# Optimization experiments

Hardware: AMD Instinct MI355X
Metric: run time of the kernel (lower is better)

Reference implementation:

```python
import jax, jax.numpy as jnp
import numpy as np

N_NODES = 100000
N_EDGES = 1600000
H, D, DE = 4, 32, 32  # heads, node_out_feats, edge_out_feats
NEG_SLOPE = 0.2


def setup_inputs() -> dict:
    key = jax.random.key(0)
    ks = jax.random.split(key, 10)
    return {
        "node_inputs": jax.random.normal(ks[0], (N_NODES, 128), jnp.float32),
        "edge_inputs": jax.random.normal(ks[1], (N_EDGES, 16), jnp.float32),
        "src": jax.random.randint(ks[2], (N_EDGES,), 0, N_NODES, jnp.int32),
        "dst": jax.random.randint(ks[3], (N_EDGES,), 0, N_NODES, jnp.int32),
        "W_fc": jax.random.normal(ks[4], (128, H * D), jnp.float32) * 0.1,
        "attn_src_p": jax.random.normal(ks[5], (1, H, D), jnp.float32) * 0.1,
        "attn_dst_p": jax.random.normal(ks[6], (1, H, D), jnp.float32) * 0.1,
        "W_edge": jax.random.normal(ks[7], (16, H * DE), jnp.float32) * 0.1,
        "attn_edge_p": jax.random.normal(ks[8], (1, H, DE), jnp.float32) * 0.1,
        "W_res": jax.random.normal(ks[9], (128, H * D), jnp.float32) * 0.1,
        "bias_p": jnp.zeros((H * D,), jnp.float32),
    }


def reference(node_inputs, edge_inputs, src, dst, W_fc, attn_src_p,
              attn_dst_p, W_edge, attn_edge_p, W_res, bias_p):
    N = node_inputs.shape[0]
    # node projection: [N, H, D]
    feat = (node_inputs @ W_fc).reshape(N, H, D)
    # per-node attention logits [N, H]
    a_src = (feat * attn_src_p).sum(-1)
    a_dst = (feat * attn_dst_p).sum(-1)
    # edge-feature attention logits [E, H]
    feat_e = (edge_inputs @ W_edge).reshape(-1, H, DE)
    a_edge = (feat_e * attn_edge_p).sum(-1)
    # per-edge score: u_add_v + edge term, then LeakyReLU
    e = a_src[src] + a_dst[dst] + a_edge                 # [E, H]
    e = jnp.where(e > 0, e, NEG_SLOPE * e)
    # edge softmax grouped by destination node
    emax = jax.lax.stop_gradient(jax.ops.segment_max(e, dst, num_segments=N))
    ex = jnp.exp(e - emax[dst])
    denom = jax.ops.segment_sum(ex, dst, num_segments=N)
    attn = ex / denom[dst]                               # [E, H]
    # weighted scatter-aggregate of source features
    msg = feat[src] * attn[:, :, None]                   # [E, H, D]
    x = jax.ops.segment_sum(msg, dst, num_segments=N)    # [N, H, D]
    # residual + bias
    x = x + (node_inputs @ W_res).reshape(N, H, D)
    x = x + bias_p.reshape(H, D)
    return x
```

## Files before the change

kernel.cpp:

```cpp
#include <hip/hip_runtime.h>
#include <math.h>

#define NNODES_FEAT 128
#define HD 128
#define H 4
#define D 32
#define EDGE_F 16
#define NEG_SLOPE 0.2f

typedef _Float16 f16;
typedef _Float16 f16x2 __attribute__((ext_vector_type(2)));
typedef _Float16 f16x4 __attribute__((ext_vector_type(4)));
typedef _Float16 f16x8 __attribute__((ext_vector_type(8)));
typedef float f32x4 __attribute__((ext_vector_type(4)));

union ExPack { float2 f; f16x4 h; };

__global__ void k_wedge(const float* __restrict__ W_edge,
                        const float* __restrict__ attn_edge,
                        float* __restrict__ w_eh) {
    int t = threadIdx.x;
    int k = t >> 2;
    int h = t & 3;
    float s = 0.f;
    for (int d = 0; d < D; ++d)
        s += W_edge[k * HD + h * D + d] * attn_edge[h * D + d];
    w_eh[k * H + h] = s;
}

__global__ __launch_bounds__(256) void k_wt(const float* __restrict__ Wfc,
                                            const float* __restrict__ Wres,
                                            f16* __restrict__ Wt) {
    int i = blockIdx.x * 256 + threadIdx.x;
    int n = i >> 7, k = i & 127;
    float v = (n < 128) ? Wfc[k * HD + n] : Wres[k * HD + (n - 128)];
    Wt[(size_t)n * 128 + k] = (f16)v;
}

#define LDK 136
__global__ __launch_bounds__(256) void k_gemm_mfma(
    const float* __restrict__ A, const f16* __restrict__ Wt,
    const float* __restrict__ bias, f16* __restrict__ feat16,
    float* __restrict__ out, int N) {
    __shared__ f16 As[64 * LDK];
    __shared__ f16 Bs[128 * LDK];
    int tid = threadIdx.x;
    int wave = tid >> 6, lane = tid & 63;
    int m0 = blockIdx.x * 64;

    for (int c = tid; c < 64 * 32; c += 256) {
        int r = c >> 5, cc = (c & 31) * 4;
        int gr = m0 + r;
        float4 v = make_float4(0.f, 0.f, 0.f, 0.f);
        if (gr < N) v = *(const float4*)(A + (size_t)gr * 128 + cc);
        f16x4 h = {(f16)v.x, (f16)v.y, (f16)v.z, (f16)v.w};
        *(f16x4*)(&As[r * LDK + cc]) = h;
    }

    int am = lane & 15, aq = lane >> 4;
    int arow = wave * 16 + am;
    int orow0 = m0 + wave * 16 + aq * 4;

    for (int cb = 0; cb < 2; ++cb) {
        if (cb) __syncthreads();
        const f16* Wblk = Wt + (size_t)cb * 128 * 128;
        for (int c = tid; c < 128 * 16; c += 256) {
            int r = c >> 4, cc = (c & 15) * 8;
            float4 v = *(const float4*)(Wblk + (size_t)r * 128 + cc);
            *(float4*)(&Bs[r * LDK + cc]) = v;
        }
        __syncthreads();

        f32x4 acc[8];
#pragma unroll
        for (int nt = 0; nt < 8; ++nt) acc[nt] = (f32x4){0.f, 0.f, 0.f, 0.f};
#pragma unroll
        for (int kc = 0; kc < 4; ++kc) {
            f16x8 a = *(const f16x8*)(&As[arow * LDK + kc * 32 + aq * 8]);
#pragma unroll
            for (int nt = 0; nt < 8; ++nt) {
                f16x8 b = *(const f16x8*)(&Bs[(nt * 16 + am) * LDK + kc * 32 + aq * 8]);
                acc[nt] = __builtin_amdgcn_mfma_f32_16x16x32_f16(a, b, acc[nt], 0, 0, 0);
            }
        }

        if (cb == 0) {
#pragma unroll
            for (int nt = 0; nt < 8; ++nt) {
                int col = nt * 16 + am;
#pragma unroll
                for (int r = 0; r < 4; ++r) {
                    int row = orow0 + r;
                    if (row < N) feat16[(size_t)row * 128 + col] = (f16)acc[nt][r];
                }
            }
        } else {
#pragma unroll
            for (int nt = 0; nt < 8; ++nt) {
                int col = nt * 16 + am;
                float bv = bias[col];
#pragma unroll
                for (int r = 0; r < 4; ++r) {
                    int row = orow0 + r;
                    if (row < N) out[(size_t)row * 128 + col] = acc[nt][r] + bv;
                }
            }
        }
    }
}

__global__ __launch_bounds__(256) void k_attn_nodes(
    const f16* __restrict__ feat16, const float* __restrict__ attn_src,
    const float* __restrict__ attn_dst, float* __restrict__ a_src,
    float* __restrict__ a_dst, int N) {
    int g = blockIdx.x * 256 + threadIdx.x;
    int n = g >> 2, h = g & 3;
    if (n >= N) return;
    const f16* f = feat16 + (size_t)n * HD + h * D;
    const float* w1 = attn_src + h * D;
    const float* w2 = attn_dst + h * D;
    float s1 = 0.f, s2 = 0.f;
#pragma unroll
    for (int dd = 0; dd < D; dd += 8) {
        f16x8 fv = *(const f16x8*)(f + dd);
#pragma unroll
        for (int j = 0; j < 8; ++j) {
            float fx = (float)fv[j];
            s1 += fx * w1[dd + j];
            s2 += fx * w2[dd + j];
        }
    }
    a_src[n * H + h] = s1;
    a_dst[n * H + h] = s2;
}

__global__ __launch_bounds__(256) void k_edge_logit(
    const float* __restrict__ edge_inputs, const int* __restrict__ src,
    const int* __restrict__ dst, const float* __restrict__ w_eh,
    const float* __restrict__ a_src, const float* __restrict__ a_dst,
    int* __restrict__ deg, int* __restrict__ rank,
    float2* __restrict__ evp, int E) {
    __shared__ float weh_s[EDGE_F * H];
    if (threadIdx.x < EDGE_F * H) weh_s[threadIdx.x] = w_eh[threadIdx.x];
    __syncthreads();

    int base = blockIdx.x * 512 + threadIdx.x;
    int e0 = base, e1 = base + 256;
    bool v0 = e0 < E, v1 = e1 < E;

    int s0 = v0 ? src[e0] : 0, s1 = v1 ? src[e1] : 0;
    int d0 = v0 ? dst[e0] : 0, d1 = v1 ? dst[e1] : 0;

    float4 xa[4], xb[4];
    if (v0) {
        const float* x = edge_inputs + (size_t)e0 * EDGE_F;
        xa[0] = *(const float4*)(x);      xa[1] = *(const float4*)(x + 4);
        xa[2] = *(const float4*)(x + 8);  xa[3] = *(const float4*)(x + 12);
    }
    if (v1) {
        const float* x = edge_inputs + (size_t)e1 * EDGE_F;
        xb[0] = *(const float4*)(x);      xb[1] = *(const float4*)(x + 4);
        xb[2] = *(const float4*)(x + 8);  xb[3] = *(const float4*)(x + 12);
    }

    float4 as0 = *(const float4*)(a_src + s0 * H);
    float4 ad0 = *(const float4*)(a_dst + d0 * H);
    float4 as1 = *(const float4*)(a_src + s1 * H);
    float4 ad1 = *(const float4*)(a_dst + d1 * H);

    int r0 = v0 ? atomicAdd(deg + d0, 1) : 0;
    int r1 = v1 ? atomicAdd(deg + d1, 1) : 0;

    if (v0) {
        float ae0 = 0.f, ae1 = 0.f, ae2 = 0.f, ae3 = 0.f;
        const float* xs = (const float*)xa;
#pragma unroll
        for (int k = 0; k < EDGE_F; ++k) {
            float xv = xs[k];
            ae0 += xv * weh_s[k * H + 0];
            ae1 += xv * weh_s[k * H + 1];
            ae2 += xv * weh_s[k * H + 2];
            ae3 += xv * weh_s[k * H + 3];
        }
        float ev[H];
        ev[0] = as0.x + ad0.x + ae0;
        ev[1] = as0.y + ad0.y + ae1;
        ev[2] = as0.z + ad0.z + ae2;
        ev[3] = as0.w + ad0.w + ae3;
#pragma unroll
        for (int h = 0; h < H; ++h) {
            float t = ev[h];
            t = t > 0.f ? t : NEG_SLOPE * t;
            ev[h] = __expf(t);
        }
        ExPack p;
        p.h = (f16x4){(f16)ev[0], (f16)ev[1], (f16)ev[2], (f16)ev[3]};
        evp[e0] = p.f;
        rank[e0] = r0;
    }
    if (v1) {
        float ae0 = 0.f, ae1 = 0.f, ae2 = 0.f, ae3 = 0.f;
        const float* xs = (const float*)xb;
#pragma unroll
        for (int k = 0; k < EDGE_F; ++k) {
            float xv = xs[k];
            ae0 += xv * weh_s[k * H + 0];
            ae1 += xv * weh_s[k * H + 1];
            ae2 += xv * weh_s[k * H + 2];
            ae3 += xv * weh_s[k * H + 3];
        }
        float ev[H];
        ev[0] = as1.x + ad1.x + ae0;
        ev[1] = as1.y + ad1.y + ae1;
        ev[2] = as1.z + ad1.z + ae2;
        ev[3] = as1.w + ad1.w + ae3;
#pragma unroll
        for (int h = 0; h < H; ++h) {
            float t = ev[h];
            t = t > 0.f ? t : NEG_SLOPE * t;
            ev[h] = __expf(t);
        }
        ExPack p;
        p.h = (f16x4){(f16)ev[0], (f16)ev[1], (f16)ev[2], (f16)ev[3]};
        evp[e1] = p.f;
        rank[e1] = r1;
    }
}

__global__ __launch_bounds__(256) void k_scan_partial(
    const int* __restrict__ deg, int* __restrict__ partial, int N) {
    __shared__ int sdata[256];
    int t = threadIdx.x;
    int base = blockIdx.x * 1024 + t * 4;
    int s = 0;
#pragma unroll
    for (int j = 0; j < 4; ++j) { int i = base + j; if (i < N) s += deg[i]; }
    sdata[t] = s;
    __syncthreads();
    for (int off = 128; off > 0; off >>= 1) {
        if (t < off) sdata[t] += sdata[t + off];
        __syncthreads();
    }
    if (t == 0) partial[blockIdx.x] = sdata[0];
}

__global__ __launch_bounds__(256) void k_scan_top(
    int* __restrict__ partial, int* __restrict__ offs, int nb, int N) {
    __shared__ int sdata[256];
    int t = threadIdx.x;
    int v = (t < nb) ? partial[t] : 0;
    sdata[t] = v;
    __syncthreads();
    for (int off = 1; off < 256; off <<= 1) {
        int add = (t >= off) ? sdata[t - off] : 0;
        __syncthreads();
        sdata[t] += add;
        __syncthreads();
    }
    int excl = (t == 0) ? 0 : sdata[t - 1];
    if (t < nb) partial[t] = excl;
    if (t == nb - 1) offs[N] = sdata[t];
}

__global__ __launch_bounds__(256) void k_scan_final(
    int* __restrict__ deg_offs, const int* __restrict__ partial, int N) {
    __shared__ int sdata[256];
    int t = threadIdx.x;
    int base = blockIdx.x * 1024 + t * 4;
    int v[4]; int s = 0;
#pragma unroll
    for (int j = 0; j < 4; ++j) { int i = base + j; v[j] = (i < N) ? deg_offs[i] : 0; s += v[j]; }
    sdata[t] = s;
    __syncthreads();
    for (int off = 1; off < 256; off <<= 1) {
        int add = (t >= off) ? sdata[t - off] : 0;
        __syncthreads();
        sdata[t] += add;
        __syncthreads();
    }
    int excl = partial[blockIdx.x] + ((t == 0) ? 0 : sdata[t - 1]);
#pragma unroll
    for (int j = 0; j < 4; ++j) {
        int i = base + j;
        if (i < N) { deg_offs[i] = excl; excl += v[j]; }
    }
}

__global__ __launch_bounds__(256) void k_permute(
    const int* __restrict__ src, const int* __restrict__ dst,
    const int* __restrict__ rank, const float2* __restrict__ evp,
    const int* __restrict__ offs, f32x4* __restrict__ rec, int E) {
    int base = blockIdx.x * 1024 + threadIdx.x;
    int s[4], d[4], r[4]; float2 q[4]; bool v[4];
#pragma unroll
    for (int j = 0; j < 4; ++j) {
        int e = base + j * 256;
        v[j] = e < E;
        s[j] = v[j] ? src[e] : 0;
        d[j] = v[j] ? dst[e] : 0;
        r[j] = v[j] ? rank[e] : 0;
        q[j] = v[j] ? evp[e] : make_float2(0.f, 0.f);
    }
    int pos[4];
#pragma unroll
    for (int j = 0; j < 4; ++j) pos[j] = offs[d[j]] + r[j];
#pragma unroll
    for (int j = 0; j < 4; ++j) {
        if (!v[j]) continue;
        f32x4 rr;
        rr[0] = __int_as_float(s[j]);
        rr[1] = q[j].x;
        rr[2] = q[j].y;
        rr[3] = 0.f;
        __builtin_nontemporal_store(rr, &rec[pos[j]]);
    }
}

__device__ __forceinline__ float exsel(float a, float b, int hword, int hshift) {
    unsigned u = __float_as_uint(hword ? b : a);
    unsigned short us = (unsigned short)(u >> hshift);
    f16 hv;
    __builtin_memcpy(&hv, &us, 2);
    return (float)hv;
}

__global__ __launch_bounds__(256) void k_aggr(
    const f16* __restrict__ feat16, const f32x4* __restrict__ rec,
    const int* __restrict__ offs, float* __restrict__ out, int N) {
    int wave = threadIdx.x >> 6;
    int lane = threadIdx.x & 63;
    int n = blockIdx.x * 4 + wave;
    if (n >= N) return;
    int beg = offs[n], end = offs[n + 1];
    if (end <= beg) return;
    int half = lane >> 5;
    int l = lane & 31;
    int hword = (l >> 4) & 1;
    int hshift = ((l >> 3) & 1) * 16;
    size_t c0 = (size_t)l * 4;
    float num0 = 0.f, num1 = 0.f, num2 = 0.f, num3 = 0.f, den = 0.f;
    int i = beg;
    for (; i + 3 < end; i += 4) {
        f32x4 ra = __builtin_nontemporal_load(&rec[i + half]);
        f32x4 rb = __builtin_nontemporal_load(&rec[i + 2 + half]);
        int sa = __float_as_int(ra[0]), sb = __float_as_int(rb[0]);
        f16x4 fa = *(const f16x4*)(feat16 + (size_t)sa * HD + c0);
        f16x4 fb = *(const f16x4*)(feat16 + (size_t)sb * HD + c0);
        float ea = exsel(ra[1], ra[2], hword, hshift);
        float eb = exsel(rb[1], rb[2], hword, hshift);
        num0 += ea * (float)fa[0] + eb * (float)fb[0];
        num1 += ea * (float)fa[1] + eb * (float)fb[1];
        num2 += ea * (float)fa[2] + eb * (float)fb[2];
        num3 += ea * (float)fa[3] + eb * (float)fb[3];
        den  += ea + eb;
    }
    for (; i + 1 < end; i += 2) {
        f32x4 ra = __builtin_nontemporal_load(&rec[i + half]);
        int sa = __float_as_int(ra[0]);
        f16x4 fa = *(const f16x4*)(feat16 + (size_t)sa * HD + c0);
        float ea = exsel(ra[1], ra[2], hword, hshift);
        num0 += ea * (float)fa[0];
        num1 += ea * (float)fa[1];
        num2 += ea * (float)fa[2];
        num3 += ea * (float)fa[3];
        den += ea;
    }
    if (i < end) {
        f32x4 ra = __builtin_nontemporal_load(&rec[i]);
        int sa = __float_as_int(ra[0]);
        f16x4 fa = *(const f16x4*)(feat16 + (size_t)sa * HD + c0);
        float ea = half ? 0.f : exsel(ra[1], ra[2], hword, hshift);
        num0 += ea * (float)fa[0];
        num1 += ea * (float)fa[1];
        num2 += ea * (float)fa[2];
        num3 += ea * (float)fa[3];
        den += ea;
    }
    num0 += __shfl_xor(num0, 32);
    num1 += __shfl_xor(num1, 32);
    num2 += __shfl_xor(num2, 32);
    num3 += __shfl_xor(num3, 32);
    den  += __shfl_xor(den, 32);
    if (half == 0) {
        float inv = 1.f / den;
        float* o = out + (size_t)n * HD + c0;
        float4 v = *(float4*)o;
        v.x += num0 * inv;
        v.y += num1 * inv;
        v.z += num2 * inv;
        v.w += num3 * inv;
        *(float4*)o = v;
    }
}

extern "C" void kernel_launch(void* const* d_in, const int* in_sizes, int n_in,
                              void* d_out, int out_size, void* d_ws, size_t ws_size,
                              hipStream_t stream) {
    const float* node_inputs = (const float*)d_in[0];
    const float* edge_inputs = (const float*)d_in[1];
    const int*   src         = (const int*)d_in[2];
    const int*   dst         = (const int*)d_in[3];
    const float* W_fc        = (const float*)d_in[4];
    const float* attn_src_p  = (const float*)d_in[5];
    const float* attn_dst_p  = (const float*)d_in[6];
    const float* W_edge      = (const float*)d_in[7];
    const float* attn_edge_p = (const float*)d_in[8];
    const float* W_res       = (const float*)d_in[9];
    const float* bias_p      = (const float*)d_in[10];

    int N = in_sizes[0] / NNODES_FEAT;
    int E = in_sizes[2];

    float* out = (float*)d_out;

    f16*    feat16  = (f16*)d_ws;
    f32x4*  rec     = (f32x4*)(feat16 + (size_t)N * HD);
    f16*    Wt      = (f16*)(rec + (size_t)E);
    float*  a_src   = (float*)(Wt + 256 * 128);
    float*  a_dst   = a_src + (size_t)N * H;
    float*  w_eh    = a_dst + (size_t)N * H;
    int*    deg     = (int*)(w_eh + 64);
    int*    offs    = deg;
    int*    partial = deg + (N + 2);
    int*    rank    = partial + 128;
    float2* evp     = (float2*)(rank + (size_t)E);

    hipMemsetAsync(deg, 0, (size_t)(N + 2) * sizeof(int), stream);

    k_wedge<<<1, 64, 0, stream>>>(W_edge, attn_edge_p, w_eh);
    k_wt<<<(256 * 128) / 256, 256, 0, stream>>>(W_fc, W_res, Wt);

    int gb = (N + 63) / 64;
    k_gemm_mfma<<<gb, 256, 0, stream>>>(node_inputs, Wt, bias_p, feat16, out, N);

    int nb = (N * H + 255) / 256;
    k_attn_nodes<<<nb, 256, 0, stream>>>(feat16, attn_src_p, attn_dst_p, a_src, a_dst, N);

    int eb = (E + 511) / 512;
    k_edge_logit<<<eb, 256, 0, stream>>>(edge_inputs, src, dst, w_eh, a_src, a_dst,
                                         deg, rank, evp, E);

    int sb = (N + 1023) / 1024;
    k_scan_partial<<<sb, 256, 0, stream>>>(deg, partial, N);
    k_scan_top<<<1, 256, 0, stream>>>(partial, offs, sb, N);
    k_scan_final<<<sb, 256, 0, stream>>>(deg, partial, N);

    int pb = (E + 1023) / 1024;
    k_permute<<<pb, 256, 0, stream>>>(src, dst, rank, evp, offs, rec, E);

    int ab = (N + 3) / 4;
    k_aggr<<<ab, 256, 0, stream>>>(feat16, rec, offs, out, N);
}
```

Before: 485.7 us.

## Fuse node attention logits into GEMM epilogue and restructure aggregation per wave

```diff
diff --git a/kernel.cpp b/kernel.cpp
--- a/kernel.cpp
+++ b/kernel.cpp
@@ -40,7 +40,9 @@
 #define LDK 136
 __global__ __launch_bounds__(256) void k_gemm_mfma(
     const float* __restrict__ A, const f16* __restrict__ Wt,
-    const float* __restrict__ bias, f16* __restrict__ feat16,
+    const float* __restrict__ bias, const float* __restrict__ asp,
+    const float* __restrict__ adp, f16* __restrict__ feat16,
+    float* __restrict__ a_src, float* __restrict__ a_dst,
     float* __restrict__ out, int N) {
     __shared__ f16 As[64 * LDK];
     __shared__ f16 Bs[128 * LDK];
@@ -94,6 +96,42 @@
                     if (row < N) feat16[(size_t)row * 128 + col] = (f16)acc[nt][r];
                 }
             }
+            float w1v[8], w2v[8];
+#pragma unroll
+            for (int nt = 0; nt < 8; ++nt) {
+                w1v[nt] = asp[nt * 16 + am];
+                w2v[nt] = adp[nt * 16 + am];
+            }
+#pragma unroll
+            for (int r = 0; r < 4; ++r) {
+                float p1[4] = {0.f, 0.f, 0.f, 0.f};
+                float p2[4] = {0.f, 0.f, 0.f, 0.f};
+#pragma unroll
+                for (int nt = 0; nt < 8; ++nt) {
+                    int h = nt >> 1;
+                    p1[h] += acc[nt][r] * w1v[nt];
+                    p2[h] += acc[nt][r] * w2v[nt];
+                }
+#pragma unroll
+                for (int off = 1; off < 16; off <<= 1) {
+#pragma unroll
+                    for (int h = 0; h < 4; ++h) {
+                        p1[h] += __shfl_xor(p1[h], off);
+                        p2[h] += __shfl_xor(p2[h], off);
+                    }
+                }
+                int row = orow0 + r;
+                if (row < N) {
+                    if (am < 4) {
+                        float v = am == 0 ? p1[0] : am == 1 ? p1[1] : am == 2 ? p1[2] : p1[3];
+                        a_src[row * 4 + am] = v;
+                    } else if (am < 8) {
+                        int hh = am - 4;
+                        float v = hh == 0 ? p2[0] : hh == 1 ? p2[1] : hh == 2 ? p2[2] : p2[3];
+                        a_dst[row * 4 + hh] = v;
+                    }
+                }
+            }
         } else {
 #pragma unroll
             for (int nt = 0; nt < 8; ++nt) {
@@ -107,31 +145,6 @@
             }
         }
     }
-}
-
-__global__ __launch_bounds__(256) void k_attn_nodes(
-    const f16* __restrict__ feat16, const float* __restrict__ attn_src,
-    const float* __restrict__ attn_dst, float* __restrict__ a_src,
-    float* __restrict__ a_dst, int N) {
-    int g = blockIdx.x * 256 + threadIdx.x;
-    int n = g >> 2, h = g & 3;
-    if (n >= N) return;
-    const f16* f = feat16 + (size_t)n * HD + h * D;
-    const float* w1 = attn_src + h * D;
-    const float* w2 = attn_dst + h * D;
-    float s1 = 0.f, s2 = 0.f;
-#pragma unroll
-    for (int dd = 0; dd < D; dd += 8) {
-        f16x8 fv = *(const f16x8*)(f + dd);
-#pragma unroll
-        for (int j = 0; j < 8; ++j) {
-            float fx = (float)fv[j];
-            s1 += fx * w1[dd + j];
-            s2 += fx * w2[dd + j];
-        }
-    }
-    a_src[n * H + h] = s1;
-    a_dst[n * H + h] = s2;
 }
 
 __global__ __launch_bounds__(256) void k_edge_logit(
@@ -289,7 +302,7 @@
 __global__ __launch_bounds__(256) void k_permute(
     const int* __restrict__ src, const int* __restrict__ dst,
     const int* __restrict__ rank, const float2* __restrict__ evp,
-    const int* __restrict__ offs, f32x4* __restrict__ rec, int E) {
+    const int* __restrict__ offs, float4* __restrict__ rec, int E) {
     int base = blockIdx.x * 1024 + threadIdx.x;
     int s[4], d[4], r[4]; float2 q[4]; bool v[4];
 #pragma unroll
@@ -307,12 +320,12 @@
 #pragma unroll
     for (int j = 0; j < 4; ++j) {
         if (!v[j]) continue;
-        f32x4 rr;
-        rr[0] = __int_as_float(s[j]);
-        rr[1] = q[j].x;
-        rr[2] = q[j].y;
-        rr[3] = 0.f;
-        __builtin_nontemporal_store(rr, &rec[pos[j]]);
+        float4 rr;
+        rr.x = __int_as_float(s[j]);
+        rr.y = q[j].x;
+        rr.z = q[j].y;
+        rr.w = 0.f;
+        rec[pos[j]] = rr;
     }
 }
 
@@ -325,7 +338,7 @@
 }
 
 __global__ __launch_bounds__(256) void k_aggr(
-    const f16* __restrict__ feat16, const f32x4* __restrict__ rec,
+    const f16* __restrict__ feat16, const float4* __restrict__ rec,
     const int* __restrict__ offs, float* __restrict__ out, int N) {
     int wave = threadIdx.x >> 6;
     int lane = threadIdx.x & 63;
@@ -333,64 +346,42 @@
     if (n >= N) return;
     int beg = offs[n], end = offs[n + 1];
     if (end <= beg) return;
-    int half = lane >> 5;
-    int l = lane & 31;
-    int hword = (l >> 4) & 1;
-    int hshift = ((l >> 3) & 1) * 16;
-    size_t c0 = (size_t)l * 4;
-    float num0 = 0.f, num1 = 0.f, num2 = 0.f, num3 = 0.f, den = 0.f;
+    int hword = (lane >> 5) & 1;
+    int hshift = ((lane >> 4) & 1) * 16;
+    size_t c0 = (size_t)2 * lane;
+    float num0 = 0.f, num1 = 0.f, den = 0.f;
     int i = beg;
     for (; i + 3 < end; i += 4) {
-        f32x4 ra = __builtin_nontemporal_load(&rec[i + half]);
-        f32x4 rb = __builtin_nontemporal_load(&rec[i + 2 + half]);
-        int sa = __float_as_int(ra[0]), sb = __float_as_int(rb[0]);
-        f16x4 fa = *(const f16x4*)(feat16 + (size_t)sa * HD + c0);
-        f16x4 fb = *(const f16x4*)(feat16 + (size_t)sb * HD + c0);
-        float ea = exsel(ra[1], ra[2], hword, hshift);
-        float eb = exsel(rb[1], rb[2], hword, hshift);
-        num0 += ea * (float)fa[0] + eb * (float)fb[0];
-        num1 += ea * (float)fa[1] + eb * (float)fb[1];
-        num2 += ea * (float)fa[2] + eb * (float)fb[2];
-        num3 += ea * (float)fa[3] + eb * (float)fb[3];
-        den  += ea + eb;
-    }
-    for (; i + 1 < end; i += 2) {
-        f32x4 ra = __builtin_nontemporal_load(&rec[i + half]);
-        int sa = __float_as_int(ra[0]);
-        f16x4 fa = *(const f16x4*)(feat16 + (size_t)sa * HD + c0);
-        float ea = exsel(ra[1], ra[2], hword, hshift);
-        num0 += ea * (float)fa[0];
-        num1 += ea * (float)fa[1];
-        num2 += ea * (float)fa[2];
-        num3 += ea * (float)fa[3];
-        den += ea;
-    }
-    if (i < end) {
-        f32x4 ra = __builtin_nontemporal_load(&rec[i]);
-        int sa = __float_as_int(ra[0]);
-        f16x4 fa = *(const f16x4*)(feat16 + (size_t)sa * HD + c0);
-        float ea = half ? 0.f : exsel(ra[1], ra[2], hword, hshift);
-        num0 += ea * (float)fa[0];
-        num1 += ea * (float)fa[1];
-        num2 += ea * (float)fa[2];
-        num3 += ea * (float)fa[3];
-        den += ea;
-    }
-    num0 += __shfl_xor(num0, 32);
-    num1 += __shfl_xor(num1, 32);
-    num2 += __shfl_xor(num2, 32);
-    num3 += __shfl_xor(num3, 32);
-    den  += __shfl_xor(den, 32);
-    if (half == 0) {
-        float inv = 1.f / den;
-        float* o = out + (size_t)n * HD + c0;
-        float4 v = *(float4*)o;
-        v.x += num0 * inv;
-        v.y += num1 * inv;
-        v.z += num2 * inv;
-        v.w += num3 * inv;
-        *(float4*)o = v;
-    }
+        float4 r0 = rec[i], r1 = rec[i + 1], r2 = rec[i + 2], r3 = rec[i + 3];
+        int s0 = __float_as_int(r0.x), s1 = __float_as_int(r1.x);
+        int s2 = __float_as_int(r2.x), s3 = __float_as_int(r3.x);
+        f16x2 f0 = *(const f16x2*)(feat16 + (size_t)s0 * HD + c0);
+        f16x2 f1 = *(const f16x2*)(feat16 + (size_t)s1 * HD + c0);
+        f16x2 f2 = *(const f16x2*)(feat16 + (size_t)s2 * HD + c0);
+        f16x2 f3 = *(const f16x2*)(feat16 + (size_t)s3 * HD + c0);
+        float e0 = exsel(r0.y, r0.z, hword, hshift);
+        float e1 = exsel(r1.y, r1.z, hword, hshift);
+        float e2 = exsel(r2.y, r2.z, hword, hshift);
+        float e3 = exsel(r3.y, r3.z, hword, hshift);
+        num0 += e0 * (float)f0.x + e1 * (float)f1.x + e2 * (float)f2.x + e3 * (float)f3.x;
+        num1 += e0 * (float)f0.y + e1 * (float)f1.y + e2 * (float)f2.y + e3 * (float)f3.y;
+        den += e0 + e1 + e2 + e3;
+    }
+    for (; i < end; ++i) {
+        float4 r0 = rec[i];
+        int s0 = __float_as_int(r0.x);
+        f16x2 f0 = *(const f16x2*)(feat16 + (size_t)s0 * HD + c0);
+        float e0 = exsel(r0.y, r0.z, hword, hshift);
+        num0 += e0 * (float)f0.x;
+        num1 += e0 * (float)f0.y;
+        den += e0;
+    }
+    float inv = 1.f / den;
+    size_t o = (size_t)n * HD + c0;
+    float2 v = *(float2*)(out + o);
+    v.x += num0 * inv;
+    v.y += num1 * inv;
+    *(float2*)(out + o) = v;
 }
 
 extern "C" void kernel_launch(void* const* d_in, const int* in_sizes, int n_in,
@@ -414,7 +405,7 @@
     float* out = (float*)d_out;
 
     f16*    feat16  = (f16*)d_ws;
-    f32x4*  rec     = (f32x4*)(feat16 + (size_t)N * HD);
+    float4* rec     = (float4*)(feat16 + (size_t)N * HD);
     f16*    Wt      = (f16*)(rec + (size_t)E);
     float*  a_src   = (float*)(Wt + 256 * 128);
     float*  a_dst   = a_src + (size_t)N * H;
@@ -431,10 +422,8 @@
     k_wt<<<(256 * 128) / 256, 256, 0, stream>>>(W_fc, W_res, Wt);
 
     int gb = (N + 63) / 64;
-    k_gemm_mfma<<<gb, 256, 0, stream>>>(node_inputs, Wt, bias_p, feat16, out, N);
-
-    int nb = (N * H + 255) / 256;
-    k_attn_nodes<<<nb, 256, 0, stream>>>(feat16, attn_src_p, attn_dst_p, a_src, a_dst, N);
+    k_gemm_mfma<<<gb, 256, 0, stream>>>(node_inputs, Wt, bias_p, attn_src_p,
+                                        attn_dst_p, feat16, a_src, a_dst, out, N);
 
     int eb = (E + 511) / 512;
     k_edge_logit<<<eb, 256, 0, stream>>>(edge_inputs, src, dst, w_eh, a_src, a_dst,
```

Measured after the change: 446.4 us. 8.1% less time.
